# Performance work log

Measured on AMD Instinct MI355X. Metric: run time of the kernel, lower is better.

Reference implementation:

```python
import jax, jax.numpy as jnp
import numpy as np

N_NODES = 50000


def _gcn_norm(edge_index, num_nodes):
    # PyG GCNConv default: add self-loops, symmetric deg^{-1/2} normalization.
    src, dst = edge_index[0], edge_index[1]
    loops = jnp.arange(num_nodes, dtype=src.dtype)
    src = jnp.concatenate([src, loops])
    dst = jnp.concatenate([dst, loops])
    ones = jnp.ones(src.shape[0], dtype=jnp.float32)
    deg = jax.ops.segment_sum(ones, dst, num_segments=num_nodes)
    dinv = jnp.where(deg > 0, jax.lax.rsqrt(deg), 0.0)
    norm = dinv[src] * dinv[dst]  # [E + N]
    return src, dst, norm


def _gcn_layer(x, src, dst, norm, W, b, num_nodes):
    h = x @ W                                   # [N, H]
    msg = h[src] * norm[:, None]                # gather + scale, [E+N, H]
    out = jax.ops.segment_sum(msg, dst, num_segments=num_nodes)  # scatter-add
    return out + b


def setup_inputs() -> dict:
    key = jax.random.key(0)
    ks = jax.random.split(key, 8)
    d_in, d_h = 128, 128
    x = jax.random.normal(ks[0], (N_NODES, d_in), dtype=jnp.float32)
    edge_index = jax.random.randint(ks[1], (2, 800000), 0, N_NODES, dtype=jnp.int64)
    s1 = 1.0 / np.sqrt(d_in)
    s2 = 1.0 / np.sqrt(d_h)
    W1 = jax.random.normal(ks[2], (d_in, d_h), dtype=jnp.float32) * s1
    b1 = jnp.zeros((d_h,), dtype=jnp.float32)
    W2 = jax.random.normal(ks[3], (d_h, d_h), dtype=jnp.float32) * s2
    b2 = jnp.zeros((d_h,), dtype=jnp.float32)
    Wl = jax.random.normal(ks[4], (d_h, 1), dtype=jnp.float32) * s2
    bl = jnp.zeros((1,), dtype=jnp.float32)
    return {"x": x, "edge_index": edge_index, "W1": W1, "b1": b1,
            "W2": W2, "b2": b2, "Wl": Wl, "bl": bl}


def reference(x, edge_index, W1, b1, W2, b2, Wl, bl):
    n = x.shape[0]
    src, dst, norm = _gcn_norm(edge_index, n)
    h = jax.nn.relu(_gcn_layer(x, src, dst, norm, W1, b1, n))
    # dropout is identity in eval mode
    h = _gcn_layer(h, src, dst, norm, W2, b2, n)
    return jax.nn.sigmoid(h @ Wl + bl)  # [N, 1]
```

## Files before the change

kernel.cpp:

```cpp
#include <hip/hip_runtime.h>
#include <math.h>

#define NN 50000
#define NE 800000
#define DD 128
#define NPAD 50048
#define NSLICE 6256
#define ELLW 64

typedef __attribute__((ext_vector_type(8))) short bf16x8;
typedef __attribute__((ext_vector_type(4))) float f32x4;
typedef __attribute__((ext_vector_type(2))) float f32x2;

__device__ __forceinline__ int clampN(int v) {
  return v < 0 ? 0 : (v >= NN ? NN - 1 : v);
}

__device__ __forceinline__ unsigned short f2b(float f) {
  union { float f; unsigned int u; } x; x.f = f;
  unsigned int u = x.u;
  u += 0x7fffu + ((u >> 16) & 1u);
  return (unsigned short)(u >> 16);
}

__device__ __forceinline__ float blo(unsigned int v) {
  union { unsigned int u; float f; } a; a.u = v << 16; return a.f;
}
__device__ __forceinline__ float bhi(unsigned int v) {
  union { unsigned int u; float f; } a; a.u = v & 0xffff0000u; return a.f;
}


__global__ __launch_bounds__(256) void k_prep_w(
    const float* __restrict__ W1, const float* __restrict__ W2,
    const float* __restrict__ b2, const float* __restrict__ Wl,
    const float* __restrict__ bl, unsigned short* __restrict__ Wt1,
    float* __restrict__ w2l, float* __restrict__ c0b, int* __restrict__ cur) {
  __shared__ float part[2];
  if (blockIdx.x < 64) {
    int i = blockIdx.x * 256 + threadIdx.x;
    int n = i >> 7, k = i & 127;
    Wt1[i] = f2b(W1[k * DD + n]);
  } else if (blockIdx.x == 64) {
    if (threadIdx.x < DD) {
      int k = threadIdx.x;
      float acc = 0.f;
      for (int c = 0; c < DD; ++c) acc += W2[k * DD + c] * Wl[c];
      w2l[k] = acc;
      float pc = b2[k] * Wl[k];
#pragma unroll
      for (int off = 32; off > 0; off >>= 1) pc += __shfl_down(pc, off, 64);
      if ((k & 63) == 0) part[k >> 6] = pc;
      __syncthreads();
      if (k == 0) c0b[0] = part[0] + part[1] + bl[0];
    }
  } else {
    int i = (blockIdx.x - 65) * 256 + threadIdx.x;
    if (i < NN) cur[i] = 0;
  }
}


__device__ __forceinline__ void scat1(int d, int s, int lo, int hi,
                                      int* __restrict__ cur,
                                      unsigned short* __restrict__ col) {
  if (d >= lo && d < hi) {
    int pos = atomicAdd(&cur[d], 1);
    if (pos < ELLW) {
      int pp = ((pos & 7) << 3) | (pos >> 3);
      col[d * ELLW + pp] = (unsigned short)clampN(s);
    }
  }
}

__global__ __launch_bounds__(256) void k_scatter4(
    const int4* __restrict__ src4, const int4* __restrict__ dst4,
    int* __restrict__ cur, unsigned short* __restrict__ col) {
  int g = blockIdx.x & 7;
  int blk = blockIdx.x >> 3;
  int lo = g * NSLICE;
  int hi = min(lo + NSLICE, NN);
  int i = blk * 256 + threadIdx.x;
  if (i >= NE / 4) return;
  int4 d4 = dst4[i];
  d4.x = clampN(d4.x); d4.y = clampN(d4.y);
  d4.z = clampN(d4.z); d4.w = clampN(d4.w);
  bool any = (d4.x >= lo && d4.x < hi) | (d4.y >= lo && d4.y < hi) |
             (d4.z >= lo && d4.z < hi) | (d4.w >= lo && d4.w < hi);
  if (any) {
    int4 s4 = src4[i];
    scat1(d4.x, s4.x, lo, hi, cur, col);
    scat1(d4.y, s4.y, lo, hi, cur, col);
    scat1(d4.z, s4.z, lo, hi, cur, col);
    scat1(d4.w, s4.w, lo, hi, cur, col);
  }
}


__global__ __launch_bounds__(256) void k_gemm_f32(
    const float* __restrict__ x, const unsigned short* __restrict__ Wt,
    const int* __restrict__ cur, unsigned short* __restrict__ outb) {
  __shared__ char lds[16384 + 32768];
  char* Al = lds;
  char* Wl = lds + 16384;

  const int tid = threadIdx.x;
  const int row0 = blockIdx.x * 64;

  {
    const float4* src = (const float4*)x;
#pragma unroll
    for (int kk = 0; kk < 8; ++kk) {
      int idx = tid + kk * 256;
      int r = idx >> 5;
      int c4 = idx & 31;
      float4 v = make_float4(0.f, 0.f, 0.f, 0.f);
      if (row0 + r < NN) v = src[(size_t)(row0 + r) * 32 + c4];
      ushort4 u;
      u.x = f2b(v.x); u.y = f2b(v.y); u.z = f2b(v.z); u.w = f2b(v.w);
      int bo = r * 256 + c4 * 8;
      *(ushort4*)(Al + (bo ^ ((r & 7) << 4))) = u;
    }
  }
  {
    const uint4* src = (const uint4*)Wt;
    for (int idx = tid; idx < 2048; idx += 256) {
      int bo = idx * 16;
      int r = bo >> 8;
      *(uint4*)(Wl + (bo ^ ((r & 7) << 4))) = src[idx];
    }
  }
  __syncthreads();

  const int w = tid >> 6, lane = tid & 63;
  const int lr = lane & 15, lk = lane >> 4;

  bf16x8 af[4];
  {
    int ar = w * 16 + lr;
    int base = ar * 256 + lk * 16;
    int swz = (ar & 7) << 4;
#pragma unroll
    for (int k4 = 0; k4 < 4; ++k4)
      af[k4] = *(const bf16x8*)(Al + ((base + k4 * 64) ^ swz));
  }

  f32x4 accs[8];
#pragma unroll
  for (int n = 0; n < 8; ++n) {
    f32x4 acc = {0.f, 0.f, 0.f, 0.f};
    int br = n * 16 + lr;
    int bbase = br * 256 + lk * 16;
    int bswz = (br & 7) << 4;
#pragma unroll
    for (int k4 = 0; k4 < 4; ++k4) {
      bf16x8 bf = *(const bf16x8*)(Wl + ((bbase + k4 * 64) ^ bswz));
      acc = __builtin_amdgcn_mfma_f32_16x16x32_bf16(af[k4], bf, acc, 0, 0, 0);
    }
    accs[n] = acc;
  }

#pragma unroll
  for (int r = 0; r < 4; ++r) {
    int grow = row0 + w * 16 + lk * 4 + r;
    if (grow < NN) {
      float dv = rsqrtf(1.0f + (float)cur[grow]);
#pragma unroll
      for (int n = 0; n < 8; ++n)
        outb[(size_t)grow * DD + n * 16 + lr] = f2b(accs[n][r] * dv);
    }
  }
}


__device__ __forceinline__ void accp(f32x2* acc, uint4 v) {
  f32x2 a0 = {blo(v.x), bhi(v.x)};
  f32x2 a1 = {blo(v.y), bhi(v.y)};
  f32x2 a2 = {blo(v.z), bhi(v.z)};
  f32x2 a3 = {blo(v.w), bhi(v.w)};
  acc[0] += a0;
  acc[1] += a1;
  acc[2] += a2;
  acc[3] += a3;
}

__global__ __launch_bounds__(256) void k_agg_relu_proj_ell(
    const uint4* __restrict__ tpb4, const float* __restrict__ b,
    const float* __restrict__ w2l, const int* __restrict__ cur,
    const unsigned short* __restrict__ col, float* __restrict__ s_out) {
  int wid = threadIdx.x >> 6;
  int lane = threadIdx.x & 63;
  int d = blockIdx.x * 4 + wid;
  int il = lane & 7, g = lane >> 3;

  f32x2 acc[8];
#pragma unroll
  for (int j = 0; j < 8; ++j) acc[j] = (f32x2){0.f, 0.f};

  int degd = cur[d];
  int deg = min(degd, ELLW);
  int cnt = (deg + 7 - g) >> 3;
  uint4 cw = ((const uint4*)col)[d * 8 + g];
  int s0 = cw.x & 0xffff, s1 = cw.x >> 16;
  int s2 = cw.y & 0xffff, s3 = cw.y >> 16;
  int s4 = cw.z & 0xffff, s5 = cw.z >> 16;
  int s6 = cw.w & 0xffff, s7 = cw.w >> 16;

#define AGG_SLOT(J, SJ)                                          \
  if (J < cnt) {                                                 \
    uint4 v0 = tpb4[(size_t)(SJ) * 16 + il * 2];                 \
    uint4 v1 = tpb4[(size_t)(SJ) * 16 + il * 2 + 1];             \
    accp(acc, v0);                                               \
    accp(acc + 4, v1);                                           \
  }
  AGG_SLOT(0, s0) AGG_SLOT(1, s1) AGG_SLOT(2, s2) AGG_SLOT(3, s3)
  AGG_SLOT(4, s4) AGG_SLOT(5, s5) AGG_SLOT(6, s6) AGG_SLOT(7, s7)
#undef AGG_SLOT

#pragma unroll
  for (int j = 0; j < 8; ++j) {
    float ax = acc[j].x, ay = acc[j].y;
    ax += __shfl_xor(ax, 8, 64);  ay += __shfl_xor(ay, 8, 64);
    ax += __shfl_xor(ax, 16, 64); ay += __shfl_xor(ay, 16, 64);
    ax += __shfl_xor(ax, 32, 64); ay += __shfl_xor(ay, 32, 64);
    acc[j].x = ax; acc[j].y = ay;
  }
  uint4 q0 = tpb4[(size_t)d * 16 + il * 2];
  uint4 q1 = tpb4[(size_t)d * 16 + il * 2 + 1];
  accp(acc, q0);
  accp(acc + 4, q1);

  float dv = rsqrtf(1.0f + (float)degd);
  float p = 0.f;
#pragma unroll
  for (int q = 0; q < 4; ++q) {
    float4 bb = ((const float4*)b)[il * 4 + q];
    float4 ww = ((const float4*)w2l)[il * 4 + q];
    p = fmaf(fmaxf(fmaf(dv, acc[2 * q].x, bb.x), 0.f), ww.x, p);
    p = fmaf(fmaxf(fmaf(dv, acc[2 * q].y, bb.y), 0.f), ww.y, p);
    p = fmaf(fmaxf(fmaf(dv, acc[2 * q + 1].x, bb.z), 0.f), ww.z, p);
    p = fmaf(fmaxf(fmaf(dv, acc[2 * q + 1].y, bb.w), 0.f), ww.w, p);
  }
  p += __shfl_xor(p, 1, 64);
  p += __shfl_xor(p, 2, 64);
  p += __shfl_xor(p, 4, 64);
  if (lane == 0) s_out[d] = dv * p;
}


__global__ __launch_bounds__(256) void k_agg_scalar_ell(
    const float* __restrict__ s, const float* __restrict__ c0b,
    const int* __restrict__ cur, const unsigned short* __restrict__ col,
    float* __restrict__ out) {
  int wid = threadIdx.x >> 6;
  int lane = threadIdx.x & 63;
  int q = lane & 15;
  int d = blockIdx.x * 16 + wid * 4 + (lane >> 4);

  int degd = cur[d];
  int deg = min(degd, ELLW);
  float tot = 0.f;
  if (q < 8) {
    int cnt = (deg + 7 - q) >> 3;
    uint4 cw = ((const uint4*)col)[d * 8 + q];
    int s0 = cw.x & 0xffff, s1 = cw.x >> 16;
    int s2 = cw.y & 0xffff, s3 = cw.y >> 16;
    int s4 = cw.z & 0xffff, s5 = cw.z >> 16;
    int s6 = cw.w & 0xffff, s7 = cw.w >> 16;
    if (0 < cnt) tot += s[s0];
    if (1 < cnt) tot += s[s1];
    if (2 < cnt) tot += s[s2];
    if (3 < cnt) tot += s[s3];
    if (4 < cnt) tot += s[s4];
    if (5 < cnt) tot += s[s5];
    if (6 < cnt) tot += s[s6];
    if (7 < cnt) tot += s[s7];
  }
  tot += __shfl_xor(tot, 1, 64);
  tot += __shfl_xor(tot, 2, 64);
  tot += __shfl_xor(tot, 4, 64);
  tot += __shfl_xor(tot, 8, 64);
  if (q == 0) {
    float dv = rsqrtf(1.0f + (float)degd);
    float z = dv * (tot + s[d]) + c0b[0];
    out[d] = 1.f / (1.f + expf(-z));
  }
}


extern "C" void kernel_launch(void* const* d_in, const int* in_sizes, int n_in,
                              void* d_out, int out_size, void* d_ws, size_t ws_size,
                              hipStream_t stream) {
  const float* x = (const float*)d_in[0];
  const int* ei = (const int*)d_in[1];
  const float* W1 = (const float*)d_in[2];
  const float* b1 = (const float*)d_in[3];
  const float* W2 = (const float*)d_in[4];
  const float* b2 = (const float*)d_in[5];
  const float* Wl = (const float*)d_in[6];
  const float* bl = (const float*)d_in[7];
  float* out = (float*)d_out;

  char* ws = (char*)d_ws;
  size_t off = 0;
  auto alloc = [&](size_t bytes) -> char* {
    char* p = ws + off;
    off = (off + bytes + 255) & ~(size_t)255;
    return p;
  };
  int* cur = (int*)alloc(NN * sizeof(int));
  unsigned short* colell = (unsigned short*)alloc((size_t)NN * ELLW * 2);
  unsigned short* Wt1 = (unsigned short*)alloc(DD * DD * 2);
  float* w2l = (float*)alloc(DD * sizeof(float));
  float* c0b = (float*)alloc(sizeof(float));
  unsigned short* tpb = (unsigned short*)alloc((size_t)NPAD * DD * 2);
  float* sbuf = (float*)alloc(NN * sizeof(float));
  (void)ws_size;

  k_prep_w<<<65 + 196, 256, 0, stream>>>(W1, W2, b2, Wl, bl, Wt1, w2l, c0b, cur);

  k_scatter4<<<8 * 782, 256, 0, stream>>>((const int4*)ei, (const int4*)(ei + NE),
                                          cur, colell);

  k_gemm_f32<<<NPAD / 64, 256, 0, stream>>>(x, Wt1, cur, tpb);

  k_agg_relu_proj_ell<<<NN / 4, 256, 0, stream>>>((const uint4*)tpb, b1, w2l,
                                                  cur, colell, sbuf);
  k_agg_scalar_ell<<<(NN + 15) / 16, 256, 0, stream>>>(sbuf, c0b, cur, colell, out);
}
```

Measured before the change: 112.3 us.

## Fold weight prep into scatter kernel and double GEMM rows per block

Weight transposition and the W2·Wl precompute are merged into the edge-scatter kernel as extra tail blocks. The counter zeroing moves to a hipMemsetAsync, which removes one separate kernel launch. The GEMM now computes 128 rows per block instead of 64, so each W tile loaded from LDS is reused across two row tiles. That cuts the W1 LDS staging per row, at the cost of doubling LDS use and accumulator registers, which may lower occupancy.

```diff
diff --git a/kernel.cpp b/kernel.cpp
--- a/kernel.cpp
+++ b/kernel.cpp
@@ -7,6 +7,7 @@
 #define NPAD 50048
 #define NSLICE 6256
 #define ELLW 64
+#define NSB 6256
 
 typedef __attribute__((ext_vector_type(8))) short bf16x8;
 typedef __attribute__((ext_vector_type(4))) float f32x4;
@@ -28,36 +29,6 @@
 }
 __device__ __forceinline__ float bhi(unsigned int v) {
   union { unsigned int u; float f; } a; a.u = v & 0xffff0000u; return a.f;
-}
-
-
-__global__ __launch_bounds__(256) void k_prep_w(
-    const float* __restrict__ W1, const float* __restrict__ W2,
-    const float* __restrict__ b2, const float* __restrict__ Wl,
-    const float* __restrict__ bl, unsigned short* __restrict__ Wt1,
-    float* __restrict__ w2l, float* __restrict__ c0b, int* __restrict__ cur) {
-  __shared__ float part[2];
-  if (blockIdx.x < 64) {
-    int i = blockIdx.x * 256 + threadIdx.x;
-    int n = i >> 7, k = i & 127;
-    Wt1[i] = f2b(W1[k * DD + n]);
-  } else if (blockIdx.x == 64) {
-    if (threadIdx.x < DD) {
-      int k = threadIdx.x;
-      float acc = 0.f;
-      for (int c = 0; c < DD; ++c) acc += W2[k * DD + c] * Wl[c];
-      w2l[k] = acc;
-      float pc = b2[k] * Wl[k];
-#pragma unroll
-      for (int off = 32; off > 0; off >>= 1) pc += __shfl_down(pc, off, 64);
-      if ((k & 63) == 0) part[k >> 6] = pc;
-      __syncthreads();
-      if (k == 0) c0b[0] = part[0] + part[1] + bl[0];
-    }
-  } else {
-    int i = (blockIdx.x - 65) * 256 + threadIdx.x;
-    if (i < NN) cur[i] = 0;
-  }
 }
 
 
@@ -73,9 +44,34 @@
   }
 }
 
-__global__ __launch_bounds__(256) void k_scatter4(
+__global__ __launch_bounds__(256) void k_scatter_prep(
     const int4* __restrict__ src4, const int4* __restrict__ dst4,
-    int* __restrict__ cur, unsigned short* __restrict__ col) {
+    int* __restrict__ cur, unsigned short* __restrict__ col,
+    const float* __restrict__ W1, const float* __restrict__ W2,
+    const float* __restrict__ b2, const float* __restrict__ Wl,
+    const float* __restrict__ bl, unsigned short* __restrict__ Wt1,
+    float* __restrict__ w2l, float* __restrict__ c0b) {
+  __shared__ float part[2];
+  if (blockIdx.x >= NSB) {
+    int pb = blockIdx.x - NSB;
+    if (pb < 64) {
+      int i = pb * 256 + threadIdx.x;
+      int n = i >> 7, k = i & 127;
+      Wt1[i] = f2b(W1[k * DD + n]);
+    } else if (threadIdx.x < DD) {
+      int k = threadIdx.x;
+      float acc = 0.f;
+      for (int c = 0; c < DD; ++c) acc += W2[k * DD + c] * Wl[c];
+      w2l[k] = acc;
+      float pc = b2[k] * Wl[k];
+#pragma unroll
+      for (int off = 32; off > 0; off >>= 1) pc += __shfl_down(pc, off, 64);
+      if ((k & 63) == 0) part[k >> 6] = pc;
+      __syncthreads();
+      if (k == 0) c0b[0] = part[0] + part[1] + bl[0];
+    }
+    return;
+  }
   int g = blockIdx.x & 7;
   int blk = blockIdx.x >> 3;
   int lo = g * NSLICE;
@@ -100,17 +96,17 @@
 __global__ __launch_bounds__(256) void k_gemm_f32(
     const float* __restrict__ x, const unsigned short* __restrict__ Wt,
     const int* __restrict__ cur, unsigned short* __restrict__ outb) {
-  __shared__ char lds[16384 + 32768];
+  __shared__ char lds[32768 + 32768];
   char* Al = lds;
-  char* Wl = lds + 16384;
+  char* Wl = lds + 32768;
 
   const int tid = threadIdx.x;
-  const int row0 = blockIdx.x * 64;
+  const int row0 = blockIdx.x * 128;
 
   {
     const float4* src = (const float4*)x;
 #pragma unroll
-    for (int kk = 0; kk < 8; ++kk) {
+    for (int kk = 0; kk < 16; ++kk) {
       int idx = tid + kk * 256;
       int r = idx >> 5;
       int c4 = idx & 31;
@@ -135,39 +131,48 @@
   const int w = tid >> 6, lane = tid & 63;
   const int lr = lane & 15, lk = lane >> 4;
 
-  bf16x8 af[4];
-  {
-    int ar = w * 16 + lr;
+  bf16x8 af[2][4];
+#pragma unroll
+  for (int rt = 0; rt < 2; ++rt) {
+    int ar = w * 32 + rt * 16 + lr;
     int base = ar * 256 + lk * 16;
     int swz = (ar & 7) << 4;
 #pragma unroll
     for (int k4 = 0; k4 < 4; ++k4)
-      af[k4] = *(const bf16x8*)(Al + ((base + k4 * 64) ^ swz));
-  }
-
-  f32x4 accs[8];
+      af[rt][k4] = *(const bf16x8*)(Al + ((base + k4 * 64) ^ swz));
+  }
+
+  f32x4 accs[2][8];
 #pragma unroll
   for (int n = 0; n < 8; ++n) {
-    f32x4 acc = {0.f, 0.f, 0.f, 0.f};
     int br = n * 16 + lr;
     int bbase = br * 256 + lk * 16;
     int bswz = (br & 7) << 4;
-#pragma unroll
-    for (int k4 = 0; k4 < 4; ++k4) {
-      bf16x8 bf = *(const bf16x8*)(Wl + ((bbase + k4 * 64) ^ bswz));
-      acc = __builtin_amdgcn_mfma_f32_16x16x32_bf16(af[k4], bf, acc, 0, 0, 0);
-    }
-    accs[n] = acc;
-  }
-
-#pragma unroll
-  for (int r = 0; r < 4; ++r) {
-    int grow = row0 + w * 16 + lk * 4 + r;
-    if (grow < NN) {
-      float dv = rsqrtf(1.0f + (float)cur[grow]);
-#pragma unroll
-      for (int n = 0; n < 8; ++n)
-        outb[(size_t)grow * DD + n * 16 + lr] = f2b(accs[n][r] * dv);
+    bf16x8 bf[4];
+#pragma unroll
+    for (int k4 = 0; k4 < 4; ++k4)
+      bf[k4] = *(const bf16x8*)(Wl + ((bbase + k4 * 64) ^ bswz));
+#pragma unroll
+    for (int rt = 0; rt < 2; ++rt) {
+      f32x4 acc = {0.f, 0.f, 0.f, 0.f};
+#pragma unroll
+      for (int k4 = 0; k4 < 4; ++k4)
+        acc = __builtin_amdgcn_mfma_f32_16x16x32_bf16(af[rt][k4], bf[k4], acc, 0, 0, 0);
+      accs[rt][n] = acc;
+    }
+  }
+
+#pragma unroll
+  for (int rt = 0; rt < 2; ++rt) {
+#pragma unroll
+    for (int r = 0; r < 4; ++r) {
+      int grow = row0 + w * 32 + rt * 16 + lk * 4 + r;
+      if (grow < NN) {
+        float dv = rsqrtf(1.0f + (float)cur[grow]);
+#pragma unroll
+        for (int n = 0; n < 8; ++n)
+          outb[(size_t)grow * DD + n * 16 + lr] = f2b(accs[rt][n][r] * dv);
+      }
     }
   }
 }
@@ -317,12 +322,13 @@
   float* sbuf = (float*)alloc(NN * sizeof(float));
   (void)ws_size;
 
-  k_prep_w<<<65 + 196, 256, 0, stream>>>(W1, W2, b2, Wl, bl, Wt1, w2l, c0b, cur);
-
-  k_scatter4<<<8 * 782, 256, 0, stream>>>((const int4*)ei, (const int4*)(ei + NE),
-                                          cur, colell);
-
-  k_gemm_f32<<<NPAD / 64, 256, 0, stream>>>(x, Wt1, cur, tpb);
+  hipMemsetAsync(cur, 0, NN * sizeof(int), stream);
+
+  k_scatter_prep<<<NSB + 65, 256, 0, stream>>>(
+      (const int4*)ei, (const int4*)(ei + NE), cur, colell,
+      W1, W2, b2, Wl, bl, Wt1, w2l, c0b);
+
+  k_gemm_f32<<<NPAD / 128, 256, 0, stream>>>(x, Wt1, cur, tpb);
 
   k_agg_relu_proj_ell<<<NN / 4, 256, 0, stream>>>((const uint4*)tpb, b1, w2l,
                                                   cur, colell, sbuf);
```

New measurement: 109.1 us. -2.9%, faster.
